# Performance work log

Hardware: AMD Instinct MI355X
Metric: run time of the kernel (lower is better)

## Reference

```python
import jax, jax.numpy as jnp
import numpy as np

N_PAIRS = 300_000
N_CENTERS = 10_000
N_SPECIES = 4
N_PSEUDO = 4
N_RADIAL = 20
L_MAX = 3


def setup_inputs() -> dict:
    key = jax.random.key(0)
    ks = jax.random.split(key, 8)
    inp = {}
    for l in range(L_MAX + 1):
        inp[f"vec_l{l}"] = jax.random.normal(ks[l], (N_PAIRS, 2 * l + 1, N_RADIAL), dtype=jnp.float32)
    # combination_matrix: Linear(n_species -> n_pseudo, bias=False) => weight [n_pseudo, n_species]
    inp["W"] = jax.random.normal(ks[4], (N_PSEUDO, N_SPECIES), dtype=jnp.float32) / np.sqrt(N_SPECIES)
    inp["species_neighbor"] = jax.random.randint(ks[5], (N_PAIRS,), 0, N_SPECIES, dtype=jnp.int64)
    inp["density_indices"] = jax.random.randint(ks[6], (N_PAIRS,), 0, N_CENTERS, dtype=jnp.int64)
    inp["n_centers"] = N_CENTERS
    return inp


def reference(vec_l0, vec_l1, vec_l2, vec_l3, W, species_neighbor, density_indices, n_centers):
    # one-hot species of neighbor, then Linear (no bias): weights [P, n_pseudo]
    one_hot_aj = jax.nn.one_hot(species_neighbor, W.shape[1], dtype=W.dtype)
    pseudo_w = one_hot_aj @ W.T  # [P, n_pseudo]
    outs = []
    for vec in (vec_l0, vec_l1, vec_l2, vec_l3):
        # outer product: [P, 2l+1, n_radial, n_pseudo]
        src = jnp.einsum('pcn,pd->pcnd', vec, pseudo_w)
        # scatter-add over unique (structure, center) groups
        dens = jax.ops.segment_sum(src, density_indices, num_segments=n_centers)
        nc, comp, nl, npse = dens.shape
        # [n_centers, 2l+1, n_pseudo, n_radial] -> flatten (pseudo-major features)
        dens = dens.swapaxes(2, 3).reshape(nc, comp * npse * nl)
        outs.append(dens)
    # concatenate all l-channels for a single output array
    return jnp.concatenate(outs, axis=1)
```

## Files before the change

### kernel.cpp

```cpp
#include <hip/hip_runtime.h>

#define N_PAIRS   300000
#define N_CENTERS 10000
#define N_FEAT    1280


__global__ void scatter_k(const int* __restrict__ didx, const int* __restrict__ species,
                          int* __restrict__ cursor, int* __restrict__ pairs,
                          int cap, int padc) {
    int p = blockIdx.x * blockDim.x + threadIdx.x;
    if (p < N_PAIRS) {
        int c = didx[p];
        int pos = atomicAdd(&cursor[c * padc], 1);
        if (pos < cap) pairs[c * cap + pos] = p | (species[p] << 20);
    }
}


__global__ __launch_bounds__(320) void accum_k(
    const float* __restrict__ vec0, const float* __restrict__ vec1,
    const float* __restrict__ vec2, const float* __restrict__ vec3,
    const float* __restrict__ W,
    const int* __restrict__ cursor, const int* __restrict__ pairs,
    float* __restrict__ out, int cap, int padc) {
    const int t = threadIdx.x;
    const int c = blockIdx.x;
    const int d = t & 3;
    const int u = t >> 2;

    const float4* src4; int s4len, foff;
    if (u < 5)       { src4 = (const float4*)vec0; s4len = 5;  foff = u;      }
    else if (u < 20) { src4 = (const float4*)vec1; s4len = 15; foff = u - 5;  }
    else if (u < 45) { src4 = (const float4*)vec2; s4len = 25; foff = u - 20; }
    else             { src4 = (const float4*)vec3; s4len = 35; foff = u - 45; }

    const int g0 = 4 * u;
    int fb, vb;
    if (g0 < 20)       { fb = 0;   vb = 0;   }
    else if (g0 < 80)  { fb = 80;  vb = 20;  }
    else if (g0 < 180) { fb = 320; vb = 80;  }
    else               { fb = 720; vb = 180; }
    const int rr = g0 - vb;
    const int cc = rr / 20;
    const int n0 = rr - cc * 20;
    const int f0 = fb + cc * 80 + d * 20 + n0;

    const float w0 = W[d * 4 + 0], w1 = W[d * 4 + 1];
    const float w2 = W[d * 4 + 2], w3 = W[d * 4 + 3];

    int cnt = cursor[c * padc];
    cnt = min(cnt, cap);
    const int* pb = pairs + c * cap;

    float4 acc = make_float4(0.f, 0.f, 0.f, 0.f);

    int4 pka = ((const int4*)pb)[0];
    int4 pkb = ((const int4*)pb)[1];

    #define G(pk, vv, ww, valid)                                   \
        {   int p_ = (pk) & 0xFFFFF;                               \
            p_ = min(p_, N_PAIRS - 1);                             \
            vv = src4[(long long)p_ * s4len + foff];               \
            int s_ = ((pk) >> 20) & 3;                             \
            float w_ = (s_ == 0) ? w0 : (s_ == 1) ? w1              \
                     : (s_ == 2) ? w2 : w3;                        \
            ww = (valid) ? w_ : 0.f; }

    for (int i = 0; i < cnt; i += 8) {
        const int4 ca = pka, cb = pkb;
        float4 v0, v1, v2, v3, v4, v5, v6, v7;
        float  a0, a1, a2, a3, a4, a5, a6, a7;
        const int rem = cnt - i;
        G(ca.x, v0, a0, true);
        G(ca.y, v1, a1, rem > 1);
        G(ca.z, v2, a2, rem > 2);
        G(ca.w, v3, a3, rem > 3);
        G(cb.x, v4, a4, rem > 4);
        G(cb.y, v5, a5, rem > 5);
        G(cb.z, v6, a6, rem > 6);
        G(cb.w, v7, a7, rem > 7);
        const int4* nx = (const int4*)(pb + i + 8);
        pka = nx[0];
        pkb = nx[1];
        acc.x += v0.x * a0; acc.y += v0.y * a0; acc.z += v0.z * a0; acc.w += v0.w * a0;
        acc.x += v1.x * a1; acc.y += v1.y * a1; acc.z += v1.z * a1; acc.w += v1.w * a1;
        acc.x += v2.x * a2; acc.y += v2.y * a2; acc.z += v2.z * a2; acc.w += v2.w * a2;
        acc.x += v3.x * a3; acc.y += v3.y * a3; acc.z += v3.z * a3; acc.w += v3.w * a3;
        acc.x += v4.x * a4; acc.y += v4.y * a4; acc.z += v4.z * a4; acc.w += v4.w * a4;
        acc.x += v5.x * a5; acc.y += v5.y * a5; acc.z += v5.z * a5; acc.w += v5.w * a5;
        acc.x += v6.x * a6; acc.y += v6.y * a6; acc.z += v6.z * a6; acc.w += v6.w * a6;
        acc.x += v7.x * a7; acc.y += v7.y * a7; acc.z += v7.z * a7; acc.w += v7.w * a7;
    }
    #undef G

    ((float4*)(out + (long long)c * N_FEAT))[f0 >> 2] = acc;
}

extern "C" void kernel_launch(void* const* d_in, const int* in_sizes, int n_in,
                              void* d_out, int out_size, void* d_ws, size_t ws_size,
                              hipStream_t stream) {
    const float* vec0 = (const float*)d_in[0];
    const float* vec1 = (const float*)d_in[1];
    const float* vec2 = (const float*)d_in[2];
    const float* vec3 = (const float*)d_in[3];
    const float* W    = (const float*)d_in[4];
    const int* species = (const int*)d_in[5];
    const int* didx    = (const int*)d_in[6];
    float* out = (float*)d_out;

    int cap = 256, padc = 16;
    auto need = [](int cap_, int padc_) {
        return ((size_t)N_CENTERS * padc_ + (size_t)N_CENTERS * cap_ + 32) * 4;
    };
    if (ws_size < need(256, 16)) { cap = 128; padc = 16; }
    if (ws_size < need(128, 16)) { cap = 128; padc = 1;  }
    if (ws_size < need(128, 1))  { cap = 64;  padc = 1;  }

    int* cursor = (int*)d_ws;
    int* pairs  = cursor + (size_t)N_CENTERS * padc;

    hipMemsetAsync(cursor, 0, (size_t)N_CENTERS * padc * sizeof(int), stream);
    const int nb = (N_PAIRS + 255) / 256;
    scatter_k<<<nb, 256, 0, stream>>>(didx, species, cursor, pairs, cap, padc);
    accum_k  <<<N_CENTERS, 320, 0, stream>>>(vec0, vec1, vec2, vec3, W,
                                             cursor, pairs, out, cap, padc);
}
```

Measured before the change: 431.6 us.

## Split pairs across thread groups and compute all pseudo channels per thread

Each thread now loads a float4 of input vectors once and applies all four pseudo-species weights to it. Previously four threads fetched the same float4 to compute one pseudo channel each. The per-center pair list and species weights are staged in shared memory first. Each of the four thread groups handles an interleaved subset of pairs, and the partial sums are combined with a shared-memory reduction before the store. This removes the 4x redundant gather loads, at the cost of more registers, extra LDS traffic and two barriers per block.

After: 424.2 us. No clear change (-1.7%).

```diff
diff --git a/kernel.cpp b/kernel.cpp
--- a/kernel.cpp
+++ b/kernel.cpp
@@ -23,16 +23,73 @@
     const float* __restrict__ W,
     const int* __restrict__ cursor, const int* __restrict__ pairs,
     float* __restrict__ out, int cap, int padc) {
+    __shared__ int    lds_pk[320];
+    __shared__ float4 lds_w4[320];
+    __shared__ float4 lds_red[16 * 80];
+
     const int t = threadIdx.x;
     const int c = blockIdx.x;
-    const int d = t & 3;
-    const int u = t >> 2;
+
+    int cnt = cursor[c * padc];
+    cnt = min(cnt, cap);
+
+    if (t < cnt) {
+        int pk = pairs[c * cap + t];
+        int s  = (pk >> 20) & 3;
+        lds_pk[t] = pk & 0xFFFFF;
+        lds_w4[t] = make_float4(W[s], W[4 + s], W[8 + s], W[12 + s]);
+    }
+
+    const int j = t / 80;
+    const int u = t - j * 80;
 
     const float4* src4; int s4len, foff;
     if (u < 5)       { src4 = (const float4*)vec0; s4len = 5;  foff = u;      }
     else if (u < 20) { src4 = (const float4*)vec1; s4len = 15; foff = u - 5;  }
     else if (u < 45) { src4 = (const float4*)vec2; s4len = 25; foff = u - 20; }
     else             { src4 = (const float4*)vec3; s4len = 35; foff = u - 45; }
+
+    float4 a0 = make_float4(0.f, 0.f, 0.f, 0.f);
+    float4 a1 = a0, a2 = a0, a3 = a0;
+
+    __syncthreads();
+
+    for (int i = 0; i < cnt; i += 16) {
+        float4 vv[4], ww[4];
+        #pragma unroll
+        for (int r = 0; r < 4; ++r) {
+            const int q  = i + r * 4 + j;
+            const int qq = min(q, cnt - 1);
+            const int p_ = lds_pk[qq];
+            float4 w = lds_w4[qq];
+            if (q >= cnt) w = make_float4(0.f, 0.f, 0.f, 0.f);
+            ww[r] = w;
+            vv[r] = src4[(long long)p_ * s4len + foff];
+        }
+        #pragma unroll
+        for (int r = 0; r < 4; ++r) {
+            const float4 v = vv[r], w = ww[r];
+            a0.x += v.x * w.x; a0.y += v.y * w.x; a0.z += v.z * w.x; a0.w += v.w * w.x;
+            a1.x += v.x * w.y; a1.y += v.y * w.y; a1.z += v.z * w.y; a1.w += v.w * w.y;
+            a2.x += v.x * w.z; a2.y += v.y * w.z; a2.z += v.z * w.z; a2.w += v.w * w.z;
+            a3.x += v.x * w.w; a3.y += v.y * w.w; a3.z += v.z * w.w; a3.w += v.w * w.w;
+        }
+    }
+
+    lds_red[(j * 4 + 0) * 80 + u] = a0;
+    lds_red[(j * 4 + 1) * 80 + u] = a1;
+    lds_red[(j * 4 + 2) * 80 + u] = a2;
+    lds_red[(j * 4 + 3) * 80 + u] = a3;
+    __syncthreads();
+
+    const float4 r0 = lds_red[(0 * 4 + j) * 80 + u];
+    const float4 r1 = lds_red[(1 * 4 + j) * 80 + u];
+    const float4 r2 = lds_red[(2 * 4 + j) * 80 + u];
+    const float4 r3 = lds_red[(3 * 4 + j) * 80 + u];
+    const float4 res = make_float4(r0.x + r1.x + r2.x + r3.x,
+                                   r0.y + r1.y + r2.y + r3.y,
+                                   r0.z + r1.z + r2.z + r3.z,
+                                   r0.w + r1.w + r2.w + r3.w);
 
     const int g0 = 4 * u;
     int fb, vb;
@@ -43,57 +100,9 @@
     const int rr = g0 - vb;
     const int cc = rr / 20;
     const int n0 = rr - cc * 20;
-    const int f0 = fb + cc * 80 + d * 20 + n0;
+    const int f0 = fb + cc * 80 + j * 20 + n0;
 
-    const float w0 = W[d * 4 + 0], w1 = W[d * 4 + 1];
-    const float w2 = W[d * 4 + 2], w3 = W[d * 4 + 3];
-
-    int cnt = cursor[c * padc];
-    cnt = min(cnt, cap);
-    const int* pb = pairs + c * cap;
-
-    float4 acc = make_float4(0.f, 0.f, 0.f, 0.f);
-
-    int4 pka = ((const int4*)pb)[0];
-    int4 pkb = ((const int4*)pb)[1];
-
-    #define G(pk, vv, ww, valid)                                   \
-        {   int p_ = (pk) & 0xFFFFF;                               \
-            p_ = min(p_, N_PAIRS - 1);                             \
-            vv = src4[(long long)p_ * s4len + foff];               \
-            int s_ = ((pk) >> 20) & 3;                             \
-            float w_ = (s_ == 0) ? w0 : (s_ == 1) ? w1              \
-                     : (s_ == 2) ? w2 : w3;                        \
-            ww = (valid) ? w_ : 0.f; }
-
-    for (int i = 0; i < cnt; i += 8) {
-        const int4 ca = pka, cb = pkb;
-        float4 v0, v1, v2, v3, v4, v5, v6, v7;
-        float  a0, a1, a2, a3, a4, a5, a6, a7;
-        const int rem = cnt - i;
-        G(ca.x, v0, a0, true);
-        G(ca.y, v1, a1, rem > 1);
-        G(ca.z, v2, a2, rem > 2);
-        G(ca.w, v3, a3, rem > 3);
-        G(cb.x, v4, a4, rem > 4);
-        G(cb.y, v5, a5, rem > 5);
-        G(cb.z, v6, a6, rem > 6);
-        G(cb.w, v7, a7, rem > 7);
-        const int4* nx = (const int4*)(pb + i + 8);
-        pka = nx[0];
-        pkb = nx[1];
-        acc.x += v0.x * a0; acc.y += v0.y * a0; acc.z += v0.z * a0; acc.w += v0.w * a0;
-        acc.x += v1.x * a1; acc.y += v1.y * a1; acc.z += v1.z * a1; acc.w += v1.w * a1;
-        acc.x += v2.x * a2; acc.y += v2.y * a2; acc.z += v2.z * a2; acc.w += v2.w * a2;
-        acc.x += v3.x * a3; acc.y += v3.y * a3; acc.z += v3.z * a3; acc.w += v3.w * a3;
-        acc.x += v4.x * a4; acc.y += v4.y * a4; acc.z += v4.z * a4; acc.w += v4.w * a4;
-        acc.x += v5.x * a5; acc.y += v5.y * a5; acc.z += v5.z * a5; acc.w += v5.w * a5;
-        acc.x += v6.x * a6; acc.y += v6.y * a6; acc.z += v6.z * a6; acc.w += v6.w * a6;
-        acc.x += v7.x * a7; acc.y += v7.y * a7; acc.z += v7.z * a7; acc.w += v7.w * a7;
-    }
-    #undef G
-
-    ((float4*)(out + (long long)c * N_FEAT))[f0 >> 2] = acc;
+    ((float4*)(out + (long long)c * N_FEAT))[f0 >> 2] = res;
 }
 
 extern "C" void kernel_launch(void* const* d_in, const int* in_sizes, int n_in,
```
